# Performance work log

Measured on AMD Instinct MI355X. Metric: run time of the kernel, lower is better.

The kernel has to match this reference:

```python
import jax, jax.numpy as jnp
import numpy as np


def setup_inputs() -> dict:
    key = jax.random.key(0)
    kq, kk, kv = jax.random.split(key, 3)
    B, N, D = 8, 4096, 128
    Q = jax.random.normal(kq, (B, N, D), dtype=jnp.float32)
    K = jax.random.normal(kk, (B, N, D), dtype=jnp.float32)
    V = jax.random.normal(kv, (B, N, D), dtype=jnp.float32)
    return {"Q": Q, "K": K, "V": V}


def reference(Q, K, V):
    # attention = Q @ K^T  -> [B, N, N]  (scale=None, mask=None path)
    attention = jnp.einsum('bnd,bmd->bnm', Q, K)
    attention = jax.nn.softmax(attention, axis=-1)
    # context = attention @ V -> [B, N, D]
    context = jnp.einsum('bnm,bmd->bnd', attention, V)
    return context
```

## Files before the change

### kernel.cpp

```cpp
#include <hip/hip_runtime.h>

#define NB 8
#define SEQ 4096
#define DIM 128
#define BQ 128
#define KVB 64
#define NTILES (SEQ / KVB)
#define ROUNDS (NTILES / 2)
#define IMG_BYTES 32768
#define WS_NEED ((size_t)NB * NTILES * IMG_BYTES)
#define L2E 1.44269504088896f

typedef _Float16 f16x8 __attribute__((ext_vector_type(8)));
typedef __bf16 bf16x8 __attribute__((ext_vector_type(8)));
typedef float f32x4 __attribute__((ext_vector_type(4)));
typedef float f32x16 __attribute__((ext_vector_type(16)));

struct U4 { unsigned x, y, z, w; };

static __device__ __forceinline__ unsigned cvtpk_bf16(float a, float b) {
  unsigned d;
  asm("v_cvt_pk_bf16_f32 %0, %1, %2" : "=v"(d) : "v"(a), "v"(b));
  return d;
}

__global__ void prep_kv(const float* __restrict__ K, const float* __restrict__ V,
                        unsigned char* __restrict__ ws) {
  const int t = blockIdx.x;
  const int b = blockIdx.y;
  unsigned char* img = ws + ((size_t)b * NTILES + t) * IMG_BYTES;
  int4* kimg = (int4*)img;
  int4* vimg = (int4*)(img + 16384);
  const float* Kb = K + ((size_t)b * SEQ + t * KVB) * DIM;
  const float* Vb = V + ((size_t)b * SEQ + t * KVB) * DIM;
  const int tid = threadIdx.x;

#pragma unroll
  for (int p = 0; p < 4; ++p) {
    const int un = tid + 256 * p;
    const int kv = un >> 4;
    const int u = (un & 15) ^ (kv & 7);
    const int s = u >> 1, hh = u & 1;
    const float* src = Kb + (size_t)kv * DIM + 16 * s + 8 * hh;
    f16x8 hv;
#pragma unroll
    for (int j = 0; j < 8; ++j) hv[j] = (_Float16)src[j];
    kimg[un] = __builtin_bit_cast(int4, hv);
  }

#pragma unroll
  for (int p = 0; p < 4; ++p) {
    const int un = tid + 256 * p;
    const int d = un >> 3;
    const int u = (un & 7) ^ (d & 7);
    const int s2 = u >> 1, hh = u & 1;
    bf16x8 hv;
#pragma unroll
    for (int e = 0; e < 8; ++e) {
      const int kv = 16 * s2 + 4 * hh + (e & 3) + 8 * (e >> 2);
      hv[e] = (__bf16)Vb[(size_t)kv * DIM + d];
    }
    vimg[un] = __builtin_bit_cast(int4, hv);
  }
}

__global__ __launch_bounds__(512, 2)
void attn_fwd6(const float* __restrict__ Q, const unsigned char* __restrict__ ws,
               float* __restrict__ O) {
  __shared__ __align__(16) unsigned char smem[131072];

  const int tid = threadIdx.x;
  const int grp = tid >> 8;
  const int w4 = (tid >> 6) & 3;
  const int l = tid & 63;
  const int l31 = l & 31;
  const int h = l >> 5;

  const int bid = blockIdx.x;
  const int b = bid & 7;
  const int qt = bid >> 3;
  const size_t base = (size_t)b * SEQ * DIM;
  const int qrow = qt * BQ + w4 * 32 + l31;

  f16x8 qf[8];
  {
    const float* qp = Q + base + (size_t)qrow * DIM + 8 * h;
#pragma unroll
    for (int s = 0; s < 8; ++s) {
      f32x4 a = *(const f32x4*)(qp + 16 * s);
      f32x4 c = *(const f32x4*)(qp + 16 * s + 4);
      f16x8 hv;
#pragma unroll
      for (int j = 0; j < 4; ++j) {
        hv[j] = (_Float16)(a[j] * L2E);
        hv[j + 4] = (_Float16)(c[j] * L2E);
      }
      qf[s] = hv;
    }
  }

  f32x16 o[4];
#pragma unroll
  for (int j = 0; j < 4; ++j) {
#pragma unroll
    for (int r = 0; r < 16; ++r) o[j][r] = 0.f;
  }
  float ls = 0.f;

  unsigned char* mybuf = smem + grp * 65536;
  const unsigned char* wsb = ws + (size_t)b * NTILES * IMG_BYTES;

  auto STAGE = [&](int t, int bufsel) {
    const unsigned char* src = wsb + (size_t)t * IMG_BYTES + w4 * 8192 + l * 16;
    unsigned char* dst = mybuf + bufsel * 32768 + w4 * 8192;
#pragma unroll
    for (int i = 0; i < 8; ++i) {
      __builtin_amdgcn_global_load_lds(
          (const __attribute__((address_space(1))) unsigned int*)(src + i * 1024),
          (__attribute__((address_space(3))) unsigned int*)(dst + i * 1024),
          16, 0, 0);
    }
  };

  const int kb2 = (l31 * 256 + ((l & 7) * 16)) ^ (h * 16);
  const int vb2 = (16384 + l31 * 128 + ((l & 7) * 16)) ^ (h * 16);

  STAGE(grp, 0);
  __syncthreads();

  for (int i = 0; i < ROUNDS; ++i) {
    const int cur = i & 1;
    if (i + 1 < ROUNDS) STAGE(2 * (i + 1) + grp, cur ^ 1);
    const unsigned char* bufp = mybuf + cur * 32768;

    f32x16 s0, s1;
#pragma unroll
    for (int r = 0; r < 16; ++r) { s0[r] = 0.f; s1[r] = 0.f; }
#pragma unroll
    for (int s = 0; s < 8; ++s) {
      const unsigned char* ka = bufp + (kb2 ^ (32 * s));
      f16x8 k0 = *(const f16x8*)(ka);
      f16x8 k1 = *(const f16x8*)(ka + 8192);
      s0 = __builtin_amdgcn_mfma_f32_32x32x16_f16(k0, qf[s], s0, 0, 0, 0);
      s1 = __builtin_amdgcn_mfma_f32_32x32x16_f16(k1, qf[s], s1, 0, 0, 0);
    }

    float a0 = 0.f, a1 = 0.f, a2 = 0.f, a3 = 0.f;
#pragma unroll
    for (int r = 0; r < 16; r += 4) {
      s0[r + 0] = exp2f(s0[r + 0]);
      s0[r + 1] = exp2f(s0[r + 1]);
      s0[r + 2] = exp2f(s0[r + 2]);
      s0[r + 3] = exp2f(s0[r + 3]);
      a0 += s0[r + 0]; a1 += s0[r + 1]; a2 += s0[r + 2]; a3 += s0[r + 3];
    }
#pragma unroll
    for (int r = 0; r < 16; r += 4) {
      s1[r + 0] = exp2f(s1[r + 0]);
      s1[r + 1] = exp2f(s1[r + 1]);
      s1[r + 2] = exp2f(s1[r + 2]);
      s1[r + 3] = exp2f(s1[r + 3]);
      a0 += s1[r + 0]; a1 += s1[r + 1]; a2 += s1[r + 2]; a3 += s1[r + 3];
    }
    ls += (a0 + a1) + (a2 + a3);

    bf16x8 pb[2][2];
#pragma unroll
    for (int u = 0; u < 2; ++u) {
      U4 t0 = {cvtpk_bf16(s0[8 * u + 0], s0[8 * u + 1]),
               cvtpk_bf16(s0[8 * u + 2], s0[8 * u + 3]),
               cvtpk_bf16(s0[8 * u + 4], s0[8 * u + 5]),
               cvtpk_bf16(s0[8 * u + 6], s0[8 * u + 7])};
      U4 t1 = {cvtpk_bf16(s1[8 * u + 0], s1[8 * u + 1]),
               cvtpk_bf16(s1[8 * u + 2], s1[8 * u + 3]),
               cvtpk_bf16(s1[8 * u + 4], s1[8 * u + 5]),
               cvtpk_bf16(s1[8 * u + 6], s1[8 * u + 7])};
      pb[0][u] = __builtin_bit_cast(bf16x8, t0);
      pb[1][u] = __builtin_bit_cast(bf16x8, t1);
    }

#pragma unroll
    for (int s2 = 0; s2 < 4; ++s2) {
      const unsigned char* va = bufp + (vb2 ^ (32 * s2));
      const bf16x8 pbb = pb[s2 >> 1][s2 & 1];
#pragma unroll
      for (int j = 0; j < 4; ++j) {
        bf16x8 vf = *(const bf16x8*)(va + j * 4096);
        o[j] = __builtin_amdgcn_mfma_f32_32x32x16_bf16(vf, pbb, o[j], 0, 0, 0);
      }
    }
    __syncthreads();
  }

  ls += __shfl_xor(ls, 32);

  if (grp == 1) {
    int4* park = (int4*)(smem + w4 * 16384);
#pragma unroll
    for (int j = 0; j < 4; ++j) {
#pragma unroll
      for (int rq = 0; rq < 4; ++rq) {
        f32x4 part = {o[j][4 * rq + 0], o[j][4 * rq + 1], o[j][4 * rq + 2],
                      o[j][4 * rq + 3]};
        park[l * 16 + ((4 * j + rq) ^ (l & 7))] = __builtin_bit_cast(int4, part);
      }
    }
    if (h == 0) *(float*)(smem + 65536 + w4 * 128 + l31 * 4) = ls;
  }
  __syncthreads();

  if (grp == 0) {
    const float lsB = *(const float*)(smem + 65536 + w4 * 128 + l31 * 4);
    const float inv = 1.0f / (ls + lsB);
    const int4* park = (const int4*)(smem + w4 * 16384);
    float* Ob = O + base + (size_t)qrow * DIM;
#pragma unroll
    for (int j = 0; j < 4; ++j) {
#pragma unroll
      for (int rq = 0; rq < 4; ++rq) {
        const f32x4 ob =
            __builtin_bit_cast(f32x4, park[l * 16 + ((4 * j + rq) ^ (l & 7))]);
        f32x4 res;
#pragma unroll
        for (int r = 0; r < 4; ++r)
          res[r] = (o[j][4 * rq + r] + ob[r]) * inv;
        *(f32x4*)(Ob + 32 * j + 8 * rq + 4 * h) = res;
      }
    }
  }
}

extern "C" void kernel_launch(void* const* d_in, const int* in_sizes, int n_in,
                              void* d_out, int out_size, void* d_ws,
                              size_t ws_size, hipStream_t stream) {
  const float* Q = (const float*)d_in[0];
  const float* K = (const float*)d_in[1];
  const float* V = (const float*)d_in[2];
  float* Out = (float*)d_out;
  if (ws_size < WS_NEED) return;
  prep_kv<<<dim3(NTILES, NB), dim3(256), 0, stream>>>(K, V, (unsigned char*)d_ws);
  attn_fwd6<<<dim3(SEQ / BQ * NB), dim3(512), 0, stream>>>(
      Q, (const unsigned char*)d_ws, Out);
}
```

Baseline: 101.2 us.

## Stream V fragments directly from global into registers, triple-buffer K in LDS

```diff
diff --git a/kernel.cpp b/kernel.cpp
--- a/kernel.cpp
+++ b/kernel.cpp
@@ -51,9 +51,11 @@
 #pragma unroll
   for (int p = 0; p < 4; ++p) {
     const int un = tid + 256 * p;
-    const int d = un >> 3;
-    const int u = (un & 7) ^ (d & 7);
-    const int s2 = u >> 1, hh = u & 1;
+    const int n = un >> 6;
+    const int l = un & 63;
+    const int s2 = n >> 2, j = n & 3;
+    const int d = 32 * j + (l & 31);
+    const int hh = l >> 5;
     bf16x8 hv;
 #pragma unroll
     for (int e = 0; e < 8; ++e) {
@@ -65,9 +67,9 @@
 }
 
 __global__ __launch_bounds__(512, 2)
-void attn_fwd6(const float* __restrict__ Q, const unsigned char* __restrict__ ws,
+void attn_fwd7(const float* __restrict__ Q, const unsigned char* __restrict__ ws,
                float* __restrict__ O) {
-  __shared__ __align__(16) unsigned char smem[131072];
+  __shared__ __align__(16) unsigned char smem[98304];
 
   const int tid = threadIdx.x;
   const int grp = tid >> 8;
@@ -107,35 +109,45 @@
   }
   float ls = 0.f;
 
-  unsigned char* mybuf = smem + grp * 65536;
+  unsigned char* mybuf = smem + grp * 49152;
   const unsigned char* wsb = ws + (size_t)b * NTILES * IMG_BYTES;
 
-  auto STAGE = [&](int t, int bufsel) {
-    const unsigned char* src = wsb + (size_t)t * IMG_BYTES + w4 * 8192 + l * 16;
-    unsigned char* dst = mybuf + bufsel * 32768 + w4 * 8192;
-#pragma unroll
-    for (int i = 0; i < 8; ++i) {
+  auto STAGE = [&](int t, int slot) {
+    const unsigned char* src = wsb + (size_t)t * IMG_BYTES + w4 * 4096 + l * 16;
+    unsigned char* dst = mybuf + slot * 16384 + w4 * 4096;
+#pragma unroll
+    for (int i2 = 0; i2 < 4; ++i2) {
       __builtin_amdgcn_global_load_lds(
-          (const __attribute__((address_space(1))) unsigned int*)(src + i * 1024),
-          (__attribute__((address_space(3))) unsigned int*)(dst + i * 1024),
+          (const __attribute__((address_space(1))) unsigned int*)(src + i2 * 1024),
+          (__attribute__((address_space(3))) unsigned int*)(dst + i2 * 1024),
           16, 0, 0);
     }
   };
 
   const int kb2 = (l31 * 256 + ((l & 7) * 16)) ^ (h * 16);
-  const int vb2 = (16384 + l31 * 128 + ((l & 7) * 16)) ^ (h * 16);
 
   STAGE(grp, 0);
-  __syncthreads();
+  STAGE(2 + grp, 1);
+  asm volatile("s_waitcnt vmcnt(4)" ::: "memory");
+  __builtin_amdgcn_s_barrier();
+  __builtin_amdgcn_sched_barrier(0);
 
   for (int i = 0; i < ROUNDS; ++i) {
-    const int cur = i & 1;
-    if (i + 1 < ROUNDS) STAGE(2 * (i + 1) + grp, cur ^ 1);
-    const unsigned char* bufp = mybuf + cur * 32768;
+    const int cur = i % 3;
+    const unsigned char* bufp = mybuf + cur * 16384;
+    const unsigned char* vtile =
+        wsb + (size_t)(2 * i + grp) * IMG_BYTES + 16384 + l * 16;
+
+    bf16x8 v01[8];
+#pragma unroll
+    for (int n = 0; n < 8; ++n) v01[n] = *(const bf16x8*)(vtile + n * 1024);
+
+    if (i + 2 < ROUNDS) STAGE(2 * (i + 2) + grp, (i + 2) % 3);
 
     f32x16 s0, s1;
 #pragma unroll
     for (int r = 0; r < 16; ++r) { s0[r] = 0.f; s1[r] = 0.f; }
+    __builtin_amdgcn_s_setprio(1);
 #pragma unroll
     for (int s = 0; s < 8; ++s) {
       const unsigned char* ka = bufp + (kb2 ^ (32 * s));
@@ -144,6 +156,12 @@
       s0 = __builtin_amdgcn_mfma_f32_32x32x16_f16(k0, qf[s], s0, 0, 0, 0);
       s1 = __builtin_amdgcn_mfma_f32_32x32x16_f16(k1, qf[s], s1, 0, 0, 0);
     }
+    __builtin_amdgcn_s_setprio(0);
+
+    bf16x8 v23[8];
+#pragma unroll
+    for (int n = 0; n < 8; ++n)
+      v23[n] = *(const bf16x8*)(vtile + (8 + n) * 1024);
 
     float a0 = 0.f, a1 = 0.f, a2 = 0.f, a3 = 0.f;
 #pragma unroll
@@ -179,20 +197,38 @@
       pb[1][u] = __builtin_bit_cast(bf16x8, t1);
     }
 
-#pragma unroll
-    for (int s2 = 0; s2 < 4; ++s2) {
-      const unsigned char* va = bufp + (vb2 ^ (32 * s2));
-      const bf16x8 pbb = pb[s2 >> 1][s2 & 1];
-#pragma unroll
-      for (int j = 0; j < 4; ++j) {
-        bf16x8 vf = *(const bf16x8*)(va + j * 4096);
-        o[j] = __builtin_amdgcn_mfma_f32_32x32x16_bf16(vf, pbb, o[j], 0, 0, 0);
-      }
-    }
-    __syncthreads();
+    __builtin_amdgcn_s_setprio(1);
+#pragma unroll
+    for (int s2 = 0; s2 < 2; ++s2) {
+      const bf16x8 pbb = pb[0][s2];
+#pragma unroll
+      for (int j = 0; j < 4; ++j)
+        o[j] = __builtin_amdgcn_mfma_f32_32x32x16_bf16(v01[4 * s2 + j], pbb,
+                                                       o[j], 0, 0, 0);
+    }
+#pragma unroll
+    for (int s2 = 0; s2 < 2; ++s2) {
+      const bf16x8 pbb = pb[1][s2];
+#pragma unroll
+      for (int j = 0; j < 4; ++j)
+        o[j] = __builtin_amdgcn_mfma_f32_32x32x16_bf16(v23[4 * s2 + j], pbb,
+                                                       o[j], 0, 0, 0);
+    }
+    __builtin_amdgcn_s_setprio(0);
+
+    if (i + 1 < ROUNDS) {
+      if (i + 2 < ROUNDS)
+        asm volatile("s_waitcnt vmcnt(4)" ::: "memory");
+      else
+        asm volatile("s_waitcnt vmcnt(0)" ::: "memory");
+      __builtin_amdgcn_s_barrier();
+      __builtin_amdgcn_sched_barrier(0);
+    }
   }
 
   ls += __shfl_xor(ls, 32);
+
+  __syncthreads();
 
   if (grp == 1) {
     int4* park = (int4*)(smem + w4 * 16384);
@@ -239,6 +275,6 @@
   float* Out = (float*)d_out;
   if (ws_size < WS_NEED) return;
   prep_kv<<<dim3(NTILES, NB), dim3(256), 0, stream>>>(K, V, (unsigned char*)d_ws);
-  attn_fwd6<<<dim3(SEQ / BQ * NB), dim3(512), 0, stream>>>(
+  attn_fwd7<<<dim3(SEQ / BQ * NB), dim3(512), 0, stream>>>(
       Q, (const unsigned char*)d_ws, Out);
 }
```

New measurement: 106.0 us. 1.05x slower.
